# Kernel optimization log

Hardware: AMD Instinct MI355X
Metric: run time of the kernel (lower is better)

Reference implementation:

```python
import jax, jax.numpy as jnp
import numpy as np

SEQ, WORD, EMBED, NHEAD = 2048, 1024, 128, 16


def setup_inputs() -> dict:
    key = jax.random.key(0)
    ks = jax.random.split(key, 6)
    sw = 1.0 / np.sqrt(WORD)  # xavier-ish scale for linear weights
    sp = 1.0 / np.sqrt(EMBED * NHEAD)
    return {
        "x": jax.random.normal(ks[0], (SEQ, WORD), jnp.float32),
        "Wq": jax.random.normal(ks[1], (NHEAD, WORD, EMBED), jnp.float32) * sw,
        "bq": jnp.zeros((NHEAD, EMBED), jnp.float32),
        "Wk": jax.random.normal(ks[2], (NHEAD, WORD, EMBED), jnp.float32) * sw,
        "bk": jnp.zeros((NHEAD, EMBED), jnp.float32),
        "Wv": jax.random.normal(ks[3], (NHEAD, WORD, EMBED), jnp.float32) * sw,
        "bv": jnp.zeros((NHEAD, EMBED), jnp.float32),
        "proj": jax.random.normal(ks[4], (NHEAD * EMBED, EMBED), jnp.float32) * sp,
    }


def reference(x, Wq, bq, Wk, bk, Wv, bv, proj):
    # Batched-head equivalent of the per-head Attention ModuleList loop.
    # x: [S, W]; Wq/Wk/Wv: [H, W, E]; b*: [H, E]; proj: [H*E, E]
    Q = jnp.einsum("sw,hwe->hse", x, Wq) + bq[:, None, :]
    K = jnp.einsum("sw,hwe->hse", x, Wk) + bk[:, None, :]
    V = jnp.einsum("sw,hwe->hse", x, Wv) + bv[:, None, :]
    scale = 1.0 / jnp.sqrt(jnp.asarray(EMBED, x.dtype))
    scores = jnp.einsum("hqe,hke->hqk", Q, K) * scale  # [H, S, S]
    attn = jax.nn.softmax(scores, axis=-1)
    Z = jnp.einsum("hqk,hke->hqe", attn, V)  # [H, S, E]
    # torch.cat([...], dim=1): per-head outputs side-by-side -> [S, H*E]
    Z_s = jnp.transpose(Z, (1, 0, 2)).reshape(x.shape[0], -1)
    return Z_s @ proj  # [S, E]
```

## Files before the change

### kernel.cpp

```cpp
#include <hip/hip_runtime.h>
#include <stdint.h>

#define GAS __attribute__((address_space(1)))
#define LAS __attribute__((address_space(3)))

typedef unsigned short u16;
typedef __attribute__((ext_vector_type(8))) __bf16 bf16x8;
typedef __attribute__((ext_vector_type(4))) float f32x4;
typedef __attribute__((ext_vector_type(4))) unsigned short u16x4;

#define SEQ 2048
#define WORD 1024
#define EMBED 128
#define NHEAD 16

__device__ __forceinline__ u16 f2b(float f) {
  return __builtin_bit_cast(u16, (__bf16)f);
}

__device__ __forceinline__ long qfrag_off(int row, int e) {
  return ((((long)(row >> 4)) * 4 + (e >> 5)) * 64 + ((e >> 3) & 3) * 16 +
          (row & 15)) * 8 + (e & 7);
}
__device__ __forceinline__ long vfrag_off(int er, int key) {
  return (((((long)(key >> 5)) * 8) + (er >> 4)) * 64 +
          ((key >> 3) & 3) * 16 + (er & 15)) * 8 + (key & 7);
}

__global__ __launch_bounds__(256) void cast_x_kernel(const float* __restrict__ x,
                                                     u16* __restrict__ xb) {
  int i = (blockIdx.x * 256 + threadIdx.x) * 4;
  float4 v = *(const float4*)(x + i);
  ushort4 o;
  o.x = f2b(v.x); o.y = f2b(v.y); o.z = f2b(v.z); o.w = f2b(v.w);
  *(ushort4*)(xb + i) = o;
}

__global__ __launch_bounds__(256) void transpose_cast_kernel(
    const float* __restrict__ s0, const float* __restrict__ s1,
    const float* __restrict__ s2, u16* __restrict__ d0, u16* __restrict__ d1,
    u16* __restrict__ d2, int R, int C, long stride, int zsel) {
  __shared__ float tile[32][33];
  const float* s;
  u16* d;
  if (zsel) {
    int z = blockIdx.z;
    int wsel = z >> 4, hh = z & 15;
    s = (wsel == 0 ? s0 : wsel == 1 ? s1 : s2) + (long)hh * stride;
    d = (wsel == 0 ? d0 : wsel == 1 ? d1 : d2) + (long)hh * stride;
  } else {
    s = s0; d = d0;
  }
  int r0 = blockIdx.x * 32, c0 = blockIdx.y * 32;
  int tx = threadIdx.x & 31, ty = threadIdx.x >> 5;
#pragma unroll
  for (int i = 0; i < 4; ++i)
    tile[ty + i * 8][tx] = s[(long)(r0 + ty + i * 8) * C + c0 + tx];
  __syncthreads();
#pragma unroll
  for (int i = 0; i < 4; ++i)
    d[(long)(c0 + ty + i * 8) * R + r0 + tx] = f2b(tile[tx][ty + i * 8]);
}

template <int MODE>
__device__ __forceinline__ void gemm128(const u16* __restrict__ A, const u16* __restrict__ B,
                                        void* __restrict__ Cp, int lda, int ldb, int ldc,
                                        int ksteps, const float* biasN, const float* biasM,
                                        float scale, int rowbase, int colbase) {
  __shared__ u16 lA[128 * 64];
  __shared__ u16 lB[128 * 64];
  const int tid = threadIdx.x;
  const int l = tid & 63, w = tid >> 6;
  const int quad = l >> 4, ln = l & 15;
  const int wm = w >> 1, wn = w & 1;
  f32x4 acc[4][4] = {};
  for (int ks = 0; ks < ksteps; ++ks) {
    const u16* Ak = A + ks * 64;
    const u16* Bk = B + ks * 64;
    __syncthreads();
#pragma unroll
    for (int i = 0; i < 4; ++i) {
      int idx = w * 256 + i * 64 + l;
      int r = idx >> 3, cp = idx & 7;
      int cg = cp ^ (r & 7);
      __builtin_amdgcn_global_load_lds((const GAS void*)(Ak + (long)r * lda + cg * 8),
                                       (LAS void*)(lA + (w * 256 + i * 64) * 8), 16, 0, 0);
      __builtin_amdgcn_global_load_lds((const GAS void*)(Bk + (long)r * ldb + cg * 8),
                                       (LAS void*)(lB + (w * 256 + i * 64) * 8), 16, 0, 0);
    }
    __syncthreads();
    bf16x8 af[2][4], bfv[2][4];
#pragma unroll
    for (int kc = 0; kc < 2; ++kc) {
#pragma unroll
      for (int i = 0; i < 4; ++i) {
        int c = kc * 4 + quad;
        int rm = wm * 64 + i * 16 + ln;
        af[kc][i] = *(const bf16x8*)(lA + rm * 64 + ((c ^ (rm & 7)) * 8));
        int rn = wn * 64 + i * 16 + ln;
        bfv[kc][i] = *(const bf16x8*)(lB + rn * 64 + ((c ^ (rn & 7)) * 8));
      }
    }
#pragma unroll
    for (int kc = 0; kc < 2; ++kc)
#pragma unroll
      for (int i = 0; i < 4; ++i)
#pragma unroll
        for (int j = 0; j < 4; ++j)
          acc[i][j] = __builtin_amdgcn_mfma_f32_16x16x32_bf16(af[kc][i], bfv[kc][j],
                                                              acc[i][j], 0, 0, 0);
  }
#pragma unroll
  for (int i = 0; i < 4; ++i) {
#pragma unroll
    for (int j = 0; j < 4; ++j) {
      int row0 = wm * 64 + i * 16 + quad * 4;
      int col = wn * 64 + j * 16 + ln;
      float bn = biasN ? biasN[col] : 0.f;
#pragma unroll
      for (int reg = 0; reg < 4; ++reg) {
        int row = row0 + reg;
        float bm = biasM ? biasM[row] : 0.f;
        float v = (acc[i][j][reg] + bn + bm) * scale;
        if constexpr (MODE == 0) {
          ((float*)Cp)[(long)row * ldc + col] = v;
        } else if constexpr (MODE == 1) {
          ((u16*)Cp)[(long)row * ldc + col] = f2b(v);
        } else if constexpr (MODE == 2) {
          ((u16*)Cp)[qfrag_off(rowbase + row, colbase + col)] = f2b(v);
        } else {
          ((u16*)Cp)[vfrag_off(rowbase + row, colbase + col)] = f2b(v);
        }
      }
    }
  }
}

__global__ __launch_bounds__(256, 3) void qkv_gemm_kernel(
    const u16* __restrict__ xb, const u16* __restrict__ Wqt, const u16* __restrict__ Wkt,
    const u16* __restrict__ Wvt, const float* __restrict__ bq, const float* __restrict__ bk,
    const float* __restrict__ bv, u16* __restrict__ Qf, u16* __restrict__ Kf,
    u16* __restrict__ Vf) {
  const int t = blockIdx.x;
  const int h = blockIdx.y;
  const int which = blockIdx.z;
  const float qscale = 0.12753042123789493f;
  if (which == 0) {
    gemm128<2>(xb + t * 128 * WORD, Wqt + h * EMBED * WORD,
               Qf + (long)h * 262144, WORD, WORD, 0,
               WORD / 64, bq + h * EMBED, nullptr, qscale, t * 128, 0);
  } else if (which == 1) {
    gemm128<2>(xb + t * 128 * WORD, Wkt + h * EMBED * WORD,
               Kf + (long)h * 262144, WORD, WORD, 0,
               WORD / 64, bk + h * EMBED, nullptr, 1.f, t * 128, 0);
  } else {
    gemm128<3>(Wvt + h * EMBED * WORD, xb + t * 128 * WORD,
               Vf + (long)h * 262144, WORD, WORD, 0,
               WORD / 64, nullptr, bv + h * EMBED, 1.f, 0, t * 128);
  }
}

__global__ __launch_bounds__(256, 2) void attn_kernel(const u16* __restrict__ Qf,
                                                      const u16* __restrict__ Kf,
                                                      const u16* __restrict__ Vf,
                                                      u16* __restrict__ Zs) {
  __shared__ char smem[34304];
  const int bid = blockIdx.x;
  const int h = bid & 15, qb = bid >> 4;
  const int tid = threadIdx.x;
  const int l = tid & 63, w = tid >> 6, quad = l >> 4, ln = l & 15;
  const int wr = w >> 1, wk = w & 1;
  const u16* Qfh = Qf + (long)h * 262144;
  u16* Pw = (u16*)smem + w * 1280;

  bf16x8 qf[2][4];
#pragma unroll
  for (int rs = 0; rs < 2; ++rs)
#pragma unroll
    for (int kc = 0; kc < 4; ++kc)
      qf[rs][kc] = *(const bf16x8*)(Qfh + (((qb * 4 + wr * 2 + rs) * 4 + kc) * 64 + l) * 8);

  const __bf16 ov = (ln == 0) ? (__bf16)1.0f : (__bf16)0.0f;
  const bf16x8 onesf = {ov, ov, ov, ov, ov, ov, ov, ov};

  f32x4 oacc[2][8] = {};
  f32x4 lacc[2] = {};

  const u16* kp = Kf + (long)h * 262144 + wk * 131072 + l * 8;
  const u16* vp = Vf + (long)h * 262144 + wk * 131072 + l * 8;

  bf16x8 kf[8], vf[8];
#pragma unroll
  for (int t = 0; t < 8; ++t) kf[t] = *(const bf16x8*)(kp + t * 512);
#pragma unroll
  for (int es = 0; es < 8; ++es) vf[es] = *(const bf16x8*)(vp + es * 512);

  for (int i = 0; i < 32; ++i) {
    f32x4 sacc[2][2] = {};
#pragma unroll
    for (int ns = 0; ns < 2; ++ns)
#pragma unroll
      for (int kc = 0; kc < 4; ++kc) {
        bf16x8 k8 = kf[ns * 4 + kc];
#pragma unroll
        for (int rs = 0; rs < 2; ++rs)
          sacc[rs][ns] = __builtin_amdgcn_mfma_f32_16x16x32_bf16(k8, qf[rs][kc],
                                                                 sacc[rs][ns], 0, 0, 0);
      }
    kp += 4096;
#pragma unroll
    for (int t = 0; t < 8; ++t) kf[t] = *(const bf16x8*)(kp + t * 512);
#pragma unroll
    for (int rs = 0; rs < 2; ++rs)
#pragma unroll
      for (int ns = 0; ns < 2; ++ns) {
        u16x4 pk;
        pk.x = f2b(exp2f(sacc[rs][ns][0]));
        pk.y = f2b(exp2f(sacc[rs][ns][1]));
        pk.z = f2b(exp2f(sacc[rs][ns][2]));
        pk.w = f2b(exp2f(sacc[rs][ns][3]));
        *(u16x4*)(Pw + (rs * 16 + ln) * 40 + (ns * 4 + quad) * 4) = pk;
      }
    bf16x8 pa[2];
#pragma unroll
    for (int rs = 0; rs < 2; ++rs)
      pa[rs] = *(const bf16x8*)(Pw + (rs * 16 + ln) * 40 + quad * 8);
#pragma unroll
    for (int es = 0; es < 8; ++es) {
      bf16x8 v8 = vf[es];
#pragma unroll
      for (int rs = 0; rs < 2; ++rs)
        oacc[rs][es] = __builtin_amdgcn_mfma_f32_16x16x32_bf16(pa[rs], v8,
                                                               oacc[rs][es], 0, 0, 0);
    }
#pragma unroll
    for (int rs = 0; rs < 2; ++rs)
      lacc[rs] = __builtin_amdgcn_mfma_f32_16x16x32_bf16(pa[rs], onesf, lacc[rs], 0, 0, 0);
    vp += 4096;
#pragma unroll
    for (int es = 0; es < 8; ++es) vf[es] = *(const bf16x8*)(vp + es * 512);
  }
  __syncthreads();
  float* lO = (float*)smem;
  float* lL = lO + 64 * 132;
  if (wk == 1) {
#pragma unroll
    for (int rs = 0; rs < 2; ++rs) {
#pragma unroll
      for (int es = 0; es < 8; ++es)
#pragma unroll
        for (int r = 0; r < 4; ++r)
          lO[(wr * 32 + rs * 16 + quad * 4 + r) * 132 + es * 16 + ln] = oacc[rs][es][r];
      if (ln == 0)
#pragma unroll
        for (int r = 0; r < 4; ++r)
          lL[wr * 32 + rs * 16 + quad * 4 + r] = lacc[rs][r];
    }
  }
  __syncthreads();
  if (wk == 0) {
#pragma unroll
    for (int rs = 0; rs < 2; ++rs)
#pragma unroll
      for (int r = 0; r < 4; ++r) {
        int grow = wr * 32 + rs * 16 + quad * 4 + r;
        float lsum = __shfl(lacc[rs][r], l & 48) + lL[grow];
        float rl = 1.f / lsum;
        int srow = qb * 64 + grow;
#pragma unroll
        for (int es = 0; es < 8; ++es) {
          float o = oacc[rs][es][r] + lO[grow * 132 + es * 16 + ln];
          Zs[(long)srow * (NHEAD * EMBED) + h * EMBED + es * 16 + ln] = f2b(o * rl);
        }
      }
  }
}

__global__ __launch_bounds__(256, 2) void final_gemm_kernel(const u16* __restrict__ Zs,
                                                            const u16* __restrict__ projT,
                                                            float* __restrict__ pbuf) {
  const int t = blockIdx.x;
  const int kc = blockIdx.y;
  gemm128<0>(Zs + (long)t * 128 * (NHEAD * EMBED) + kc * 256, projT + kc * 256,
             pbuf + (long)kc * SEQ * EMBED + t * 128 * EMBED,
             NHEAD * EMBED, NHEAD * EMBED, EMBED, 4, nullptr, nullptr, 1.f, 0, 0);
}

__global__ __launch_bounds__(256) void reduce_kernel(const float* __restrict__ pbuf,
                                                     float* __restrict__ out) {
  int i = (blockIdx.x * 256 + threadIdx.x) * 4;
  float4 s = {0.f, 0.f, 0.f, 0.f};
#pragma unroll
  for (int kc = 0; kc < 8; ++kc) {
    float4 v = *(const float4*)(pbuf + (long)kc * SEQ * EMBED + i);
    s.x += v.x; s.y += v.y; s.z += v.z; s.w += v.w;
  }
  *(float4*)(out + i) = s;
}

extern "C" void kernel_launch(void* const* d_in, const int* in_sizes, int n_in,
                              void* d_out, int out_size, void* d_ws, size_t ws_size,
                              hipStream_t stream) {
  const float* x    = (const float*)d_in[0];
  const float* Wq   = (const float*)d_in[1];
  const float* bq   = (const float*)d_in[2];
  const float* Wk   = (const float*)d_in[3];
  const float* bk   = (const float*)d_in[4];
  const float* Wv   = (const float*)d_in[5];
  const float* bv   = (const float*)d_in[6];
  const float* proj = (const float*)d_in[7];
  float* out = (float*)d_out;

  char* ws = (char*)d_ws;
  u16* xb    = (u16*)(ws);
  u16* Wqt   = (u16*)(ws + (4L << 20));
  u16* Wkt   = (u16*)(ws + (8L << 20));
  u16* Wvt   = (u16*)(ws + (12L << 20));
  u16* projT = (u16*)(ws + (16L << 20));
  u16* Qf    = (u16*)(ws + (17L << 20));
  u16* Kf    = (u16*)(ws + (26L << 20));
  u16* Vf    = (u16*)(ws + (35L << 20));
  u16* Zs    = (u16*)(ws + (44L << 20));
  float* pbuf = (float*)(ws);

  cast_x_kernel<<<dim3(SEQ * WORD / 1024), dim3(256), 0, stream>>>(x, xb);
  transpose_cast_kernel<<<dim3(WORD / 32, EMBED / 32, 48), dim3(256), 0, stream>>>(
      Wq, Wk, Wv, Wqt, Wkt, Wvt, WORD, EMBED, (long)WORD * EMBED, 1);
  transpose_cast_kernel<<<dim3(SEQ / 32, EMBED / 32, 1), dim3(256), 0, stream>>>(
      proj, nullptr, nullptr, projT, nullptr, nullptr, SEQ, EMBED, 0, 0);

  qkv_gemm_kernel<<<dim3(16, NHEAD, 3), dim3(256), 0, stream>>>(
      xb, Wqt, Wkt, Wvt, bq, bk, bv, Qf, Kf, Vf);

  attn_kernel<<<dim3(512), dim3(256), 0, stream>>>(Qf, Kf, Vf, Zs);

  final_gemm_kernel<<<dim3(16, 8), dim3(256), 0, stream>>>(Zs, projT, pbuf);
  reduce_kernel<<<dim3(SEQ * EMBED / 1024), dim3(256), 0, stream>>>(pbuf, out);
}
```

Before: 210.3 us.

## Split attention keys across four waves and merge prep kernels into one launch

The attention kernel now uses 512 threads per block, so each row group has four waves that each cover a quarter of the keys instead of half. Their partial outputs and row sums are combined through shared memory in three serialized accumulate steps. The goal is more waves per CU to hide load and MFMA latency, at the cost of a longer reduction and higher register pressure under the 512-thread launch bound. Separately, the x cast and the weight and proj transpose-casts are folded into one prep kernel to save two launches.

```diff
diff --git a/kernel.cpp b/kernel.cpp
--- a/kernel.cpp
+++ b/kernel.cpp
@@ -27,35 +27,45 @@
           ((key >> 3) & 3) * 16 + (er & 15)) * 8 + (key & 7);
 }
 
-__global__ __launch_bounds__(256) void cast_x_kernel(const float* __restrict__ x,
-                                                     u16* __restrict__ xb) {
-  int i = (blockIdx.x * 256 + threadIdx.x) * 4;
-  float4 v = *(const float4*)(x + i);
-  ushort4 o;
-  o.x = f2b(v.x); o.y = f2b(v.y); o.z = f2b(v.z); o.w = f2b(v.w);
-  *(ushort4*)(xb + i) = o;
-}
-
-__global__ __launch_bounds__(256) void transpose_cast_kernel(
-    const float* __restrict__ s0, const float* __restrict__ s1,
-    const float* __restrict__ s2, u16* __restrict__ d0, u16* __restrict__ d1,
-    u16* __restrict__ d2, int R, int C, long stride, int zsel) {
+__global__ __launch_bounds__(256) void prep_kernel(
+    const float* __restrict__ x, const float* __restrict__ Wq,
+    const float* __restrict__ Wk, const float* __restrict__ Wv,
+    const float* __restrict__ proj, u16* __restrict__ xb, u16* __restrict__ Wqt,
+    u16* __restrict__ Wkt, u16* __restrict__ Wvt, u16* __restrict__ projT) {
+  int b = blockIdx.x;
+  if (b < 2048) {
+    int i = b * 1024 + threadIdx.x * 4;
+    float4 v = *(const float4*)(x + i);
+    ushort4 o;
+    o.x = f2b(v.x); o.y = f2b(v.y); o.z = f2b(v.z); o.w = f2b(v.w);
+    *(ushort4*)(xb + i) = o;
+    return;
+  }
   __shared__ float tile[32][33];
   const float* s;
   u16* d;
-  if (zsel) {
-    int z = blockIdx.z;
+  int R, r0, c0;
+  if (b < 8192) {
+    int idx = b - 2048;
+    int z = idx >> 7, t2 = idx & 127;
     int wsel = z >> 4, hh = z & 15;
-    s = (wsel == 0 ? s0 : wsel == 1 ? s1 : s2) + (long)hh * stride;
-    d = (wsel == 0 ? d0 : wsel == 1 ? d1 : d2) + (long)hh * stride;
+    long off = (long)hh * WORD * EMBED;
+    s = (wsel == 0 ? Wq : wsel == 1 ? Wk : Wv) + off;
+    d = (wsel == 0 ? Wqt : wsel == 1 ? Wkt : Wvt) + off;
+    R = WORD;
+    r0 = (t2 & 31) * 32;
+    c0 = (t2 >> 5) * 32;
   } else {
-    s = s0; d = d0;
-  }
-  int r0 = blockIdx.x * 32, c0 = blockIdx.y * 32;
+    int idx = b - 8192;
+    s = proj; d = projT;
+    R = SEQ;
+    r0 = (idx & 63) * 32;
+    c0 = (idx >> 6) * 32;
+  }
   int tx = threadIdx.x & 31, ty = threadIdx.x >> 5;
 #pragma unroll
   for (int i = 0; i < 4; ++i)
-    tile[ty + i * 8][tx] = s[(long)(r0 + ty + i * 8) * C + c0 + tx];
+    tile[ty + i * 8][tx] = s[(long)(r0 + ty + i * 8) * EMBED + c0 + tx];
   __syncthreads();
 #pragma unroll
   for (int i = 0; i < 4; ++i)
@@ -160,7 +170,7 @@
   }
 }
 
-__global__ __launch_bounds__(256, 2) void attn_kernel(const u16* __restrict__ Qf,
+__global__ __launch_bounds__(512, 2) void attn_kernel(const u16* __restrict__ Qf,
                                                       const u16* __restrict__ Kf,
                                                       const u16* __restrict__ Vf,
                                                       u16* __restrict__ Zs) {
@@ -169,7 +179,7 @@
   const int h = bid & 15, qb = bid >> 4;
   const int tid = threadIdx.x;
   const int l = tid & 63, w = tid >> 6, quad = l >> 4, ln = l & 15;
-  const int wr = w >> 1, wk = w & 1;
+  const int wr = w >> 2, wk = w & 3;
   const u16* Qfh = Qf + (long)h * 262144;
   u16* Pw = (u16*)smem + w * 1280;
 
@@ -186,16 +196,22 @@
   f32x4 oacc[2][8] = {};
   f32x4 lacc[2] = {};
 
-  const u16* kp = Kf + (long)h * 262144 + wk * 131072 + l * 8;
-  const u16* vp = Vf + (long)h * 262144 + wk * 131072 + l * 8;
+  const u16* kp = Kf + (long)h * 262144 + wk * 65536 + l * 8;
+  const u16* vp = Vf + (long)h * 262144 + wk * 65536 + l * 8;
+  const u16* kp4 = kp + 2048;
+  const u16* vp4 = vp + 2048;
 
   bf16x8 kf[8], vf[8];
 #pragma unroll
-  for (int t = 0; t < 8; ++t) kf[t] = *(const bf16x8*)(kp + t * 512);
-#pragma unroll
-  for (int es = 0; es < 8; ++es) vf[es] = *(const bf16x8*)(vp + es * 512);
-
-  for (int i = 0; i < 32; ++i) {
+  for (int t = 0; t < 4; ++t) kf[t] = *(const bf16x8*)(kp + t * 512);
+#pragma unroll
+  for (int t = 0; t < 4; ++t) kf[t + 4] = *(const bf16x8*)(kp4 + t * 512);
+#pragma unroll
+  for (int t = 0; t < 4; ++t) vf[t] = *(const bf16x8*)(vp + t * 512);
+#pragma unroll
+  for (int t = 0; t < 4; ++t) vf[t + 4] = *(const bf16x8*)(vp4 + t * 512);
+
+  for (int i = 0; i < 16; ++i) {
     f32x4 sacc[2][2] = {};
 #pragma unroll
     for (int ns = 0; ns < 2; ++ns)
@@ -207,9 +223,11 @@
           sacc[rs][ns] = __builtin_amdgcn_mfma_f32_16x16x32_bf16(k8, qf[rs][kc],
                                                                  sacc[rs][ns], 0, 0, 0);
       }
-    kp += 4096;
-#pragma unroll
-    for (int t = 0; t < 8; ++t) kf[t] = *(const bf16x8*)(kp + t * 512);
+    kp += 4096; kp4 += 4096;
+#pragma unroll
+    for (int t = 0; t < 4; ++t) kf[t] = *(const bf16x8*)(kp + t * 512);
+#pragma unroll
+    for (int t = 0; t < 4; ++t) kf[t + 4] = *(const bf16x8*)(kp4 + t * 512);
 #pragma unroll
     for (int rs = 0; rs < 2; ++rs)
 #pragma unroll
@@ -236,28 +254,38 @@
 #pragma unroll
     for (int rs = 0; rs < 2; ++rs)
       lacc[rs] = __builtin_amdgcn_mfma_f32_16x16x32_bf16(pa[rs], onesf, lacc[rs], 0, 0, 0);
-    vp += 4096;
-#pragma unroll
-    for (int es = 0; es < 8; ++es) vf[es] = *(const bf16x8*)(vp + es * 512);
+    vp += 4096; vp4 += 4096;
+#pragma unroll
+    for (int t = 0; t < 4; ++t) vf[t] = *(const bf16x8*)(vp + t * 512);
+#pragma unroll
+    for (int t = 0; t < 4; ++t) vf[t + 4] = *(const bf16x8*)(vp4 + t * 512);
   }
   __syncthreads();
   float* lO = (float*)smem;
   float* lL = lO + 64 * 132;
-  if (wk == 1) {
-#pragma unroll
-    for (int rs = 0; rs < 2; ++rs) {
-#pragma unroll
-      for (int es = 0; es < 8; ++es)
-#pragma unroll
-        for (int r = 0; r < 4; ++r)
-          lO[(wr * 32 + rs * 16 + quad * 4 + r) * 132 + es * 16 + ln] = oacc[rs][es][r];
-      if (ln == 0)
-#pragma unroll
-        for (int r = 0; r < 4; ++r)
-          lL[wr * 32 + rs * 16 + quad * 4 + r] = lacc[rs][r];
-    }
-  }
-  __syncthreads();
+  for (int st = 3; st >= 1; --st) {
+    if (wk == st) {
+#pragma unroll
+      for (int rs = 0; rs < 2; ++rs) {
+#pragma unroll
+        for (int es = 0; es < 8; ++es)
+#pragma unroll
+          for (int r = 0; r < 4; ++r) {
+            int idx = (wr * 32 + rs * 16 + quad * 4 + r) * 132 + es * 16 + ln;
+            if (st == 3) lO[idx] = oacc[rs][es][r];
+            else lO[idx] += oacc[rs][es][r];
+          }
+        if (ln == 0)
+#pragma unroll
+          for (int r = 0; r < 4; ++r) {
+            int row = wr * 32 + rs * 16 + quad * 4 + r;
+            if (st == 3) lL[row] = lacc[rs][r];
+            else lL[row] += lacc[rs][r];
+          }
+      }
+    }
+    __syncthreads();
+  }
   if (wk == 0) {
 #pragma unroll
     for (int rs = 0; rs < 2; ++rs)
@@ -323,16 +351,13 @@
   u16* Zs    = (u16*)(ws + (44L << 20));
   float* pbuf = (float*)(ws);
 
-  cast_x_kernel<<<dim3(SEQ * WORD / 1024), dim3(256), 0, stream>>>(x, xb);
-  transpose_cast_kernel<<<dim3(WORD / 32, EMBED / 32, 48), dim3(256), 0, stream>>>(
-      Wq, Wk, Wv, Wqt, Wkt, Wvt, WORD, EMBED, (long)WORD * EMBED, 1);
-  transpose_cast_kernel<<<dim3(SEQ / 32, EMBED / 32, 1), dim3(256), 0, stream>>>(
-      proj, nullptr, nullptr, projT, nullptr, nullptr, SEQ, EMBED, 0, 0);
+  prep_kernel<<<dim3(8448), dim3(256), 0, stream>>>(x, Wq, Wk, Wv, proj, xb, Wqt,
+                                                    Wkt, Wvt, projT);
 
   qkv_gemm_kernel<<<dim3(16, NHEAD, 3), dim3(256), 0, stream>>>(
       xb, Wqt, Wkt, Wvt, bq, bk, bv, Qf, Kf, Vf);
 
-  attn_kernel<<<dim3(512), dim3(256), 0, stream>>>(Qf, Kf, Vf, Zs);
+  attn_kernel<<<dim3(512), dim3(512), 0, stream>>>(Qf, Kf, Vf, Zs);
 
   final_gemm_kernel<<<dim3(16, 8), dim3(256), 0, stream>>>(Zs, projT, pbuf);
   reduce_kernel<<<dim3(SEQ * EMBED / 1024), dim3(256), 0, stream>>>(pbuf, out);
```

Result: no change. 207.0 us (-1.6%).
